# Performance work log

Measured on AMD Instinct MI355X. Metric: run time of the kernel, lower is better.

The kernel has to match this reference:

```python
import jax, jax.numpy as jnp
import numpy as np

B, S, D = 4, 2048, 1024
H, HD = 16, 64
L = 512          # kv latent dim (MLA compression)
E, TOPK, F = 8, 2, 2048  # MoE experts / top-k / expert hidden
EPS = 1e-6


def rmsnorm(x, g):
    return x * jax.lax.rsqrt(jnp.mean(x * x, axis=-1, keepdims=True) + EPS) * g


def setup_inputs() -> dict:
    key = jax.random.key(0)
    ks = jax.random.split(key, 16)
    std = 0.02
    inp = {
        "prev_hidden": jax.random.normal(ks[0], (B, S, D), jnp.float32),
        "future_token_embed": jax.random.normal(ks[1], (B, S, D), jnp.float32),
        "w_combine": jax.random.normal(ks[2], (2 * D, D), jnp.float32) * std,
        "g1": jnp.ones((D,), jnp.float32),
        "g2": jnp.ones((D,), jnp.float32),
        "g_attn": jnp.ones((D,), jnp.float32),
        "g_mlp": jnp.ones((D,), jnp.float32),
        "wq": jax.random.normal(ks[3], (D, D), jnp.float32) * std,
        "w_dkv": jax.random.normal(ks[4], (D, L), jnp.float32) * std,
        "w_uk": jax.random.normal(ks[5], (L, D), jnp.float32) * std,
        "w_uv": jax.random.normal(ks[6], (L, D), jnp.float32) * std,
        "wo": jax.random.normal(ks[7], (D, D), jnp.float32) * std,
        "w_gate": jax.random.normal(ks[8], (D, E), jnp.float32) * std,
        "w1": jax.random.normal(ks[9], (E, D, F), jnp.float32) * std,
        "w3": jax.random.normal(ks[10], (E, D, F), jnp.float32) * std,
        "w2": jax.random.normal(ks[11], (E, F, D), jnp.float32) * std,
    }
    return inp


def mla_attention(x, wq, w_dkv, w_uk, w_uv, wo):
    # Multi-head latent attention: KV compressed through latent dim L.
    q = (x @ wq).reshape(B, S, H, HD)
    c = x @ w_dkv                       # [B,S,L] latent
    k = (c @ w_uk).reshape(B, S, H, HD)
    v = (c @ w_uv).reshape(B, S, H, HD)
    scores = jnp.einsum("bqhd,bkhd->bhqk", q, k) / jnp.sqrt(jnp.float32(HD))
    causal = jnp.tril(jnp.ones((S, S), bool))
    scores = jnp.where(causal, scores, jnp.float32(-1e9))
    attn = jax.nn.softmax(scores, axis=-1)
    out = jnp.einsum("bhqk,bkhd->bqhd", attn, v).reshape(B, S, D)
    return out @ wo


def moe(x, w_gate, w1, w3, w2):
    t = x.reshape(-1, D)                          # [T,D]
    probs = jax.nn.softmax(t @ w_gate, axis=-1)   # [T,E]
    vals, idx = jax.lax.top_k(probs, TOPK)        # [T,K]
    vals = vals / jnp.sum(vals, axis=-1, keepdims=True)
    gates = jnp.sum(vals[:, :, None] * jax.nn.one_hot(idx, E, dtype=x.dtype), axis=1)  # [T,E]
    out = jnp.zeros_like(t)
    for e in range(E):  # fixed small expert loop (structurally distinct weights)
        h = jax.nn.silu(t @ w1[e]) * (t @ w3[e])
        out = out + gates[:, e:e + 1] * (h @ w2[e])
    return out.reshape(x.shape)


def reference(prev_hidden, future_token_embed, w_combine, g1, g2, g_attn, g_mlp,
              wq, w_dkv, w_uk, w_uv, wo, w_gate, w1, w3, w2):
    prev_norm = rmsnorm(prev_hidden, g1)
    future_norm = rmsnorm(future_token_embed, g2)
    combined = jnp.concatenate([prev_norm, future_norm], axis=-1)
    hidden = combined @ w_combine
    hidden = hidden + mla_attention(rmsnorm(hidden, g_attn), wq, w_dkv, w_uk, w_uv, wo)
    hidden = hidden + moe(rmsnorm(hidden, g_mlp), w_gate, w1, w3, w2)
    return hidden
```

## Files before the change

kernel.cpp:

```cpp
#include <hip/hip_runtime.h>
#include <hip/hip_bf16.h>
#include <stdint.h>

#define B_ 4
#define S_ 2048
#define D_ 1024
#define H_ 16
#define L_ 512
#define E_ 8
#define F_ 2048
#define T_ (B_*S_)

typedef __hip_bfloat16 bf16_t;
typedef __attribute__((ext_vector_type(8))) short short8;
typedef __attribute__((ext_vector_type(4))) float f32x4;

__device__ __forceinline__ void gl2lds16(const void* g, void* l) {
  __builtin_amdgcn_global_load_lds(
      reinterpret_cast<const __attribute__((address_space(1))) void*>(reinterpret_cast<uintptr_t>(g)),
      reinterpret_cast<__attribute__((address_space(3))) void*>(reinterpret_cast<uintptr_t>(l)),
      16, 0, 0);
}
__device__ __forceinline__ unsigned short bf16u(bf16_t b) {
  return *reinterpret_cast<unsigned short*>(&b);
}
__device__ __forceinline__ void split2(float v, bf16_t& ho, bf16_t& lo) {
  ho = __float2bfloat16(v);
  lo = __float2bfloat16(v - __bfloat162float(ho));
}
__device__ __forceinline__ float bf2f(bf16_t b) { return __bfloat162float(b); }

__global__ __launch_bounds__(256) void k_fill(float* out, float code, int n) {
  int i = blockIdx.x * 256 + threadIdx.x;
  if (i < n) out[i] = (i == 0 ? code : 0.f);
}

__global__ __launch_bounds__(256) void k_transpose(const float* __restrict__ in,
                                                   bf16_t* __restrict__ out, int R, int C, int ldin,
                                                   size_t zin, size_t zout) {
  __shared__ float t[32][33];
  const float* inz = in + (size_t)blockIdx.z * zin;
  bf16_t* outz = out + (size_t)blockIdx.z * zout;
  int c0 = blockIdx.x * 32, r0 = blockIdx.y * 32;
  int tx = threadIdx.x, ty = threadIdx.y;
#pragma unroll
  for (int i = 0; i < 4; ++i)
    t[ty + 8*i][tx] = inz[(size_t)(r0 + ty + 8*i) * ldin + c0 + tx];
  __syncthreads();
#pragma unroll
  for (int i = 0; i < 4; ++i)
    outz[(size_t)(c0 + ty + 8*i) * R + r0 + tx] = __float2bfloat16(t[tx][ty + 8*i]);
}

__global__ __launch_bounds__(256) void k_transpose2(const float* __restrict__ in,
                                                    bf16_t* __restrict__ oh, bf16_t* __restrict__ ol,
                                                    int R, int C, int ldin) {
  __shared__ float t[32][33];
  int c0 = blockIdx.x * 32, r0 = blockIdx.y * 32;
  int tx = threadIdx.x, ty = threadIdx.y;
#pragma unroll
  for (int i = 0; i < 4; ++i)
    t[ty + 8*i][tx] = in[(size_t)(r0 + ty + 8*i) * ldin + c0 + tx];
  __syncthreads();
#pragma unroll
  for (int i = 0; i < 4; ++i) {
    float v = t[tx][ty + 8*i];
    size_t idx = (size_t)(c0 + ty + 8*i) * R + r0 + tx;
    bf16_t h, l; split2(v, h, l);
    oh[idx] = h; ol[idx] = l;
  }
}

__global__ __launch_bounds__(256) void k_rms2cat2(const float* __restrict__ pa, const float* __restrict__ pb,
                                                  const float* __restrict__ g1, const float* __restrict__ g2,
                                                  bf16_t* __restrict__ oh, bf16_t* __restrict__ ol) {
  const int row = blockIdx.x, tid = threadIdx.x;
  float4 a = reinterpret_cast<const float4*>(pa + (size_t)row * D_)[tid];
  float4 b = reinterpret_cast<const float4*>(pb + (size_t)row * D_)[tid];
  float sa = a.x*a.x + a.y*a.y + a.z*a.z + a.w*a.w;
  float sb = b.x*b.x + b.y*b.y + b.z*b.z + b.w*b.w;
#pragma unroll
  for (int o = 32; o; o >>= 1) { sa += __shfl_xor(sa, o, 64); sb += __shfl_xor(sb, o, 64); }
  __shared__ float red[8];
  if ((tid & 63) == 0) { red[tid >> 6] = sa; red[4 + (tid >> 6)] = sb; }
  __syncthreads();
  sa = red[0] + red[1] + red[2] + red[3];
  sb = red[4] + red[5] + red[6] + red[7];
  float ra = rsqrtf(sa * (1.f / D_) + 1e-6f);
  float rb = rsqrtf(sb * (1.f / D_) + 1e-6f);
  float4 ga = reinterpret_cast<const float4*>(g1)[tid];
  float4 gb = reinterpret_cast<const float4*>(g2)[tid];
  float va[4] = {a.x*ra*ga.x, a.y*ra*ga.y, a.z*ra*ga.z, a.w*ra*ga.w};
  float vb[4] = {b.x*rb*gb.x, b.y*rb*gb.y, b.z*rb*gb.z, b.w*rb*gb.w};
  size_t base = (size_t)row * 2 * D_ + tid * 4;
#pragma unroll
  for (int j = 0; j < 4; ++j) {
    bf16_t h, l;
    split2(va[j], h, l); oh[base + j] = h; ol[base + j] = l;
    split2(vb[j], h, l); oh[base + D_ + j] = h; ol[base + D_ + j] = l;
  }
}

__global__ __launch_bounds__(256) void k_rmsnorm2(const float* __restrict__ x, const float* __restrict__ g,
                                                  bf16_t* __restrict__ oh, bf16_t* __restrict__ ol) {
  const int row = blockIdx.x, tid = threadIdx.x;
  float4 v = reinterpret_cast<const float4*>(x + (size_t)row * D_)[tid];
  float ss = v.x*v.x + v.y*v.y + v.z*v.z + v.w*v.w;
#pragma unroll
  for (int o = 32; o; o >>= 1) ss += __shfl_xor(ss, o, 64);
  __shared__ float red[4];
  if ((tid & 63) == 0) red[tid >> 6] = ss;
  __syncthreads();
  ss = red[0] + red[1] + red[2] + red[3];
  float rs = rsqrtf(ss * (1.f / D_) + 1e-6f);
  float4 gv = reinterpret_cast<const float4*>(g)[tid];
  float y[4] = {v.x*rs*gv.x, v.y*rs*gv.y, v.z*rs*gv.z, v.w*rs*gv.w};
  size_t base = (size_t)row * D_ + tid * 4;
#pragma unroll
  for (int j = 0; j < 4; ++j) {
    bf16_t h, l; split2(y[j], h, l);
    oh[base + j] = h;
    ol[base + j] = l;
  }
}

__global__ __launch_bounds__(256) void k_rmsgate(const float* __restrict__ x, const float* __restrict__ g,
                                                 const float* __restrict__ wg,
                                                 bf16_t* __restrict__ oh, float* __restrict__ gates) {
  const int row = blockIdx.x, tid = threadIdx.x;
  float4 v = reinterpret_cast<const float4*>(x + (size_t)row * D_)[tid];
  float ss = v.x*v.x + v.y*v.y + v.z*v.z + v.w*v.w;
#pragma unroll
  for (int o = 32; o; o >>= 1) ss += __shfl_xor(ss, o, 64);
  __shared__ float red[4];
  __shared__ float eacc[4][8];
  if ((tid & 63) == 0) red[tid >> 6] = ss;
  __syncthreads();
  ss = red[0] + red[1] + red[2] + red[3];
  float rs = rsqrtf(ss * (1.f / D_) + 1e-6f);
  float4 gv = reinterpret_cast<const float4*>(g)[tid];
  float y[4] = {v.x*rs*gv.x, v.y*rs*gv.y, v.z*rs*gv.z, v.w*rs*gv.w};
  size_t base = (size_t)row * D_ + tid * 4;
#pragma unroll
  for (int j = 0; j < 4; ++j) oh[base + j] = __float2bfloat16(y[j]);
  float acc[8] = {0, 0, 0, 0, 0, 0, 0, 0};
#pragma unroll
  for (int j = 0; j < 4; ++j) {
    const float* wgr = wg + (size_t)(tid * 4 + j) * 8;
#pragma unroll
    for (int e = 0; e < 8; ++e) acc[e] += y[j] * wgr[e];
  }
#pragma unroll
  for (int e = 0; e < 8; ++e) {
#pragma unroll
    for (int o = 32; o; o >>= 1) acc[e] += __shfl_xor(acc[e], o, 64);
  }
  if ((tid & 63) == 0) {
#pragma unroll
    for (int e = 0; e < 8; ++e) eacc[tid >> 6][e] = acc[e];
  }
  __syncthreads();
  if (tid == 0) {
    float a[8];
#pragma unroll
    for (int e = 0; e < 8; ++e) a[e] = eacc[0][e] + eacc[1][e] + eacc[2][e] + eacc[3][e];
    float mx = a[0];
#pragma unroll
    for (int e = 1; e < 8; ++e) mx = fmaxf(mx, a[e]);
    float p[8], sum = 0.f;
#pragma unroll
    for (int e = 0; e < 8; ++e) { p[e] = __expf(a[e] - mx); sum += p[e]; }
#pragma unroll
    for (int e = 0; e < 8; ++e) p[e] /= sum;
    int i0 = 0; float v0 = p[0];
#pragma unroll
    for (int e = 1; e < 8; ++e) if (p[e] > v0) { v0 = p[e]; i0 = e; }
    int i1 = -1; float v1 = -1.f;
#pragma unroll
    for (int e = 0; e < 8; ++e) if (e != i0 && p[e] > v1) { v1 = p[e]; i1 = e; }
    float norm = v0 + v1;
#pragma unroll
    for (int e = 0; e < 8; ++e)
      gates[(size_t)row * 8 + e] = (e == i0) ? v0 / norm : ((e == i1) ? v1 / norm : 0.f);
  }
}

__global__ __launch_bounds__(256) void k_route_det(const float* __restrict__ gates,
                                                   int* __restrict__ idx, int* __restrict__ cnt) {
  const int e = blockIdx.x, tid = threadIdx.x;
  __shared__ int sc[256];
  int base = 0;
  for (int c0 = 0; c0 < T_; c0 += 256) {
    int t = c0 + tid;
    int m = (gates[(size_t)t * 8 + e] > 0.f) ? 1 : 0;
    sc[tid] = m;
    __syncthreads();
#pragma unroll
    for (int off = 1; off < 256; off <<= 1) {
      int v = (tid >= off) ? sc[tid - off] : 0;
      __syncthreads();
      sc[tid] += v;
      __syncthreads();
    }
    if (m) idx[e * T_ + base + sc[tid] - 1] = t;
    int tot = sc[255];
    __syncthreads();
    base += tot;
  }
  if (tid == 0) cnt[e] = base;
}

__global__ void k_prefix(const int* __restrict__ cnt, int* __restrict__ off) {
  int s = 0;
  for (int e = 0; e < E_; ++e) { off[e] = s; s += cnt[e]; }
}

template <int EPI, int SPLIT, int IDX>
__global__ __launch_bounds__(256) void k_sgemm(
    const bf16_t* __restrict__ Ah, const bf16_t* __restrict__ Al,
    const bf16_t* __restrict__ Bh, const bf16_t* __restrict__ Bl,
    float* __restrict__ Cf, bf16_t* __restrict__ Cb, bf16_t* __restrict__ Cb2,
    bf16_t* __restrict__ Cb3, bf16_t* __restrict__ Cb4,
    const float* __restrict__ scale, const int* __restrict__ aidx, const int* __restrict__ cnt,
    int N, int K, int lda, int ldc) {
  __shared__ __align__(16) char lds[(SPLIT == 3 ? 4 : 2) * 16384];
  char* lsAh = lds;
  char* lsBh = lds + 16384;
  char* lsAl = lds + 32768;
  char* lsBl = lds + 49152;
  const int tid = threadIdx.x;
  const int l = tid & 63;
  const int g16 = l >> 4, c16 = l & 15;
  const int nbn = N >> 7;
  int swz = (int)blockIdx.x;
  if constexpr (IDX == 0 && EPI != 6) {
    swz = (swz & 7) * ((int)gridDim.x >> 3) + (swz >> 3);
  }
  const int bm = swz / nbn, bn = swz % nbn;
  const int m0 = bm << 7, n0 = bn << 7;
  const int w = tid >> 6;
  const int wr = w >> 1, wc = w & 1;

  int cval = 0;
  if constexpr (IDX == 1 || EPI == 6) {
    cval = *cnt;
    if (m0 >= cval) return;
  }

  f32x4 acc[4][4] = {};

  int Lb[4], sr[4], sk[4];
#pragma unroll
  for (int i = 0; i < 4; ++i) {
    Lb[i] = (tid + i * 256) * 16;
    sr[i] = Lb[i] >> 7;
    sk[i] = ((Lb[i] & 127) ^ ((sr[i] & 7) << 4)) >> 1;
  }
  int arow[4];
#pragma unroll
  for (int i = 0; i < 4; ++i) {
    if constexpr (IDX == 1) {
      int p = m0 + sr[i];
      arow[i] = aidx[p < cval ? p : cval - 1];
    } else {
      arow[i] = m0 + sr[i];
    }
  }

  for (int k0 = 0; k0 < K; k0 += 64) {
#pragma unroll
    for (int i = 0; i < 4; ++i) {
      size_t aoff = (size_t)arow[i] * lda + k0 + sk[i];
      size_t boff = (size_t)(n0 + sr[i]) * K + k0 + sk[i];
      gl2lds16(Ah + aoff, lsAh + Lb[i]);
      gl2lds16(Bh + boff, lsBh + Lb[i]);
      if constexpr (SPLIT == 3) {
        gl2lds16(Al + aoff, lsAl + Lb[i]);
        gl2lds16(Bl + boff, lsBl + Lb[i]);
      }
    }
    __syncthreads();
#pragma unroll
    for (int kc = 0; kc < 2; ++kc) {
      const int kb = (kc * 32 + 8 * g16) * 2;
      short8 afh[4], bfh[4], afl[4], bfl[4];
#pragma unroll
      for (int m = 0; m < 4; ++m) {
        int row = wr * 64 + m * 16 + c16;
        int off = row * 128 + (kb ^ ((row & 7) << 4));
        afh[m] = *reinterpret_cast<const short8*>(lsAh + off);
        if constexpr (SPLIT == 3) afl[m] = *reinterpret_cast<const short8*>(lsAl + off);
      }
#pragma unroll
      for (int n = 0; n < 4; ++n) {
        int row = wc * 64 + n * 16 + c16;
        int off = row * 128 + (kb ^ ((row & 7) << 4));
        bfh[n] = *reinterpret_cast<const short8*>(lsBh + off);
        if constexpr (SPLIT == 3) bfl[n] = *reinterpret_cast<const short8*>(lsBl + off);
      }
#pragma unroll
      for (int m = 0; m < 4; ++m)
#pragma unroll
        for (int n = 0; n < 4; ++n) {
          if constexpr (SPLIT == 3) {
            acc[m][n] = __builtin_amdgcn_mfma_f32_16x16x32_bf16(afl[m], bfh[n], acc[m][n], 0, 0, 0);
            acc[m][n] = __builtin_amdgcn_mfma_f32_16x16x32_bf16(afh[m], bfl[n], acc[m][n], 0, 0, 0);
          }
          acc[m][n] = __builtin_amdgcn_mfma_f32_16x16x32_bf16(afh[m], bfh[n], acc[m][n], 0, 0, 0);
        }
    }
    __syncthreads();
  }

#pragma unroll
  for (int m = 0; m < 4; ++m) {
    int rb = m0 + wr * 64 + m * 16 + 4 * g16;
#pragma unroll
    for (int n = 0; n < 4; ++n) {
      int gc = n0 + wc * 64 + n * 16 + c16;
#pragma unroll
      for (int r = 0; r < 4; ++r) {
        float v = acc[m][n][r];
        if constexpr (EPI == 6) {
          int rbr = rb + r;
          if (rbr < cval) {
            int tok = aidx[rbr];
            Cf[(size_t)tok * ldc + gc] += scale[(size_t)tok * 8] * v;
          }
        } else if constexpr (EPI == 7) {
          int t = rb + r;
          bf16_t h, lo; split2(v, h, lo);
          if (gc < 1024) {
            size_t ki = (size_t)t * 1024 + gc;
            Cb[ki] = h; Cb2[ki] = lo;
          } else {
            size_t vi = (size_t)(t >> 11) * 2097152 + (size_t)(gc - 1024) * 2048 + (t & 2047);
            Cb3[vi] = h; Cb4[vi] = lo;
          }
        } else {
          size_t idx = (size_t)(rb + r) * ldc + gc;
          if constexpr (EPI == 0) Cf[idx] = v;
          if constexpr (EPI == 1) Cf[idx] += v;
          if constexpr (EPI == 2) { bf16_t h, lo; split2(v, h, lo); Cb[idx] = h; Cb2[idx] = lo; }
          if constexpr (EPI == 3) Cb[idx] = __float2bfloat16(v / (1.f + __expf(-v)));
          if constexpr (EPI == 4) Cb[idx] = __float2bfloat16(bf2f(Cb[idx]) * v);
        }
      }
    }
  }
}

__global__ __launch_bounds__(256) void k_moe1(
    const bf16_t* __restrict__ xn, const bf16_t* __restrict__ w1t, const bf16_t* __restrict__ w3t,
    bf16_t* __restrict__ hg, const int* __restrict__ idx8, const int* __restrict__ cnt8,
    const int* __restrict__ off8) {
  __shared__ __align__(16) char lds[3 * 16384];
  char* lsA = lds;
  char* lsB1 = lds + 16384;
  char* lsB2 = lds + 32768;
  const int tid = threadIdx.x, l = tid & 63, g16 = l >> 4, c16 = l & 15;
  const int e = blockIdx.z;
  const int nbn = F_ >> 7;
  const int bm = (int)blockIdx.x / nbn, bn = (int)blockIdx.x % nbn;
  const int m0 = bm << 7, n0 = bn << 7;
  const int w = tid >> 6, wr = w >> 1, wc = w & 1;
  const int* aidx = idx8 + e * T_;
  const int cval = cnt8[e];
  if (m0 >= cval) return;
  const int obase = off8[e];
  const bf16_t* B1 = w1t + (size_t)e * D_ * F_;
  const bf16_t* B2 = w3t + (size_t)e * D_ * F_;

  f32x4 a1[4][4] = {}, a3[4][4] = {};
  int Lb[4], sr[4], sk[4], arow[4];
#pragma unroll
  for (int i = 0; i < 4; ++i) {
    Lb[i] = (tid + i * 256) * 16;
    sr[i] = Lb[i] >> 7;
    sk[i] = ((Lb[i] & 127) ^ ((sr[i] & 7) << 4)) >> 1;
    int p = m0 + sr[i];
    arow[i] = aidx[p < cval ? p : cval - 1];
  }
  for (int k0 = 0; k0 < D_; k0 += 64) {
#pragma unroll
    for (int i = 0; i < 4; ++i) {
      gl2lds16(xn + (size_t)arow[i] * D_ + k0 + sk[i], lsA + Lb[i]);
      size_t boff = (size_t)(n0 + sr[i]) * D_ + k0 + sk[i];
      gl2lds16(B1 + boff, lsB1 + Lb[i]);
      gl2lds16(B2 + boff, lsB2 + Lb[i]);
    }
    __syncthreads();
#pragma unroll
    for (int kc = 0; kc < 2; ++kc) {
      const int kb = (kc * 32 + 8 * g16) * 2;
      short8 af[4], b1[4], b2[4];
#pragma unroll
      for (int m = 0; m < 4; ++m) {
        int row = wr * 64 + m * 16 + c16;
        af[m] = *reinterpret_cast<const short8*>(lsA + row * 128 + (kb ^ ((row & 7) << 4)));
      }
#pragma unroll
      for (int n = 0; n < 4; ++n) {
        int row = wc * 64 + n * 16 + c16;
        int off = row * 128 + (kb ^ ((row & 7) << 4));
        b1[n] = *reinterpret_cast<const short8*>(lsB1 + off);
        b2[n] = *reinterpret_cast<const short8*>(lsB2 + off);
      }
#pragma unroll
      for (int m = 0; m < 4; ++m)
#pragma unroll
        for (int n = 0; n < 4; ++n) {
          a1[m][n] = __builtin_amdgcn_mfma_f32_16x16x32_bf16(af[m], b1[n], a1[m][n], 0, 0, 0);
          a3[m][n] = __builtin_amdgcn_mfma_f32_16x16x32_bf16(af[m], b2[n], a3[m][n], 0, 0, 0);
        }
    }
    __syncthreads();
  }
#pragma unroll
  for (int m = 0; m < 4; ++m) {
    int rb = m0 + wr * 64 + m * 16 + 4 * g16;
#pragma unroll
    for (int n = 0; n < 4; ++n) {
      int gc = n0 + wc * 64 + n * 16 + c16;
#pragma unroll
      for (int r = 0; r < 4; ++r) {
        int rbr = rb + r;
        if (rbr < cval) {
          float v1 = a1[m][n][r], v3 = a3[m][n][r];
          hg[(size_t)(obase + rbr) * F_ + gc] = __float2bfloat16(v1 / (1.f + __expf(-v1)) * v3);
        }
      }
    }
  }
}

__global__ __launch_bounds__(256) void k_moe2z(
    const bf16_t* __restrict__ hg, const bf16_t* __restrict__ w2t,
    float* __restrict__ hid, const float* __restrict__ gates,
    const int* __restrict__ idx8, const int* __restrict__ cnt8, const int* __restrict__ off8) {
  __shared__ __align__(16) char lds[2 * 16384];
  char* lsA = lds;
  char* lsB = lds + 16384;
  const int tid = threadIdx.x, l = tid & 63, g16 = l >> 4, c16 = l & 15;
  const int e = blockIdx.z;
  const int nbn = D_ >> 7;
  const int bm = (int)blockIdx.x / nbn, bn = (int)blockIdx.x % nbn;
  const int m0 = bm << 7, n0 = bn << 7;
  const int w = tid >> 6, wr = w >> 1, wc = w & 1;
  const int* aidx = idx8 + e * T_;
  const int cval = cnt8[e];
  if (m0 >= cval) return;
  const int obase = off8[e];
  const bf16_t* Bt = w2t + (size_t)e * D_ * F_;

  f32x4 acc[4][4] = {};
  int Lb[4], sr[4], sk[4];
#pragma unroll
  for (int i = 0; i < 4; ++i) {
    Lb[i] = (tid + i * 256) * 16;
    sr[i] = Lb[i] >> 7;
    sk[i] = ((Lb[i] & 127) ^ ((sr[i] & 7) << 4)) >> 1;
  }
  for (int k0 = 0; k0 < F_; k0 += 64) {
#pragma unroll
    for (int i = 0; i < 4; ++i) {
      gl2lds16(hg + (size_t)(obase + m0 + sr[i]) * F_ + k0 + sk[i], lsA + Lb[i]);
      gl2lds16(Bt + (size_t)(n0 + sr[i]) * F_ + k0 + sk[i], lsB + Lb[i]);
    }
    __syncthreads();
#pragma unroll
    for (int kc = 0; kc < 2; ++kc) {
      const int kb = (kc * 32 + 8 * g16) * 2;
      short8 af[4], bf8[4];
#pragma unroll
      for (int m = 0; m < 4; ++m) {
        int row = wr * 64 + m * 16 + c16;
        af[m] = *reinterpret_cast<const short8*>(lsA + row * 128 + (kb ^ ((row & 7) << 4)));
      }
#pragma unroll
      for (int n = 0; n < 4; ++n) {
        int row = wc * 64 + n * 16 + c16;
        bf8[n] = *reinterpret_cast<const short8*>(lsB + row * 128 + (kb ^ ((row & 7) << 4)));
      }
#pragma unroll
      for (int m = 0; m < 4; ++m)
#pragma unroll
        for (int n = 0; n < 4; ++n)
          acc[m][n] = __builtin_amdgcn_mfma_f32_16x16x32_bf16(af[m], bf8[n], acc[m][n], 0, 0, 0);
    }
    __syncthreads();
  }
#pragma unroll
  for (int m = 0; m < 4; ++m) {
    int rb = m0 + wr * 64 + m * 16 + 4 * g16;
#pragma unroll
    for (int n = 0; n < 4; ++n) {
      int gc = n0 + wc * 64 + n * 16 + c16;
#pragma unroll
      for (int r = 0; r < 4; ++r) {
        int rbr = rb + r;
        if (rbr < cval) {
          int tok = aidx[rbr];
          atomicAdd(&hid[(size_t)tok * D_ + gc], gates[(size_t)tok * 8 + e] * acc[m][n][r]);
        }
      }
    }
  }
}

__global__ __launch_bounds__(1024) void k_flash16(
    const bf16_t* __restrict__ qh, const bf16_t* __restrict__ ql,
    const bf16_t* __restrict__ kbh, const bf16_t* __restrict__ kbl,
    const bf16_t* __restrict__ vth, const bf16_t* __restrict__ vtl,
    bf16_t* __restrict__ ch, bf16_t* __restrict__ cl, int zb) {
  __shared__ __align__(16) char lds[131072];
  const int tid = threadIdx.x, l = tid & 63, w = tid >> 6;
  const int g16 = l >> 4, c16 = l & 15;
  const int qt = (int)gridDim.y - 1 - (int)blockIdx.y;
  const int h = (int)blockIdx.x / zb;
  const int z = (int)blockIdx.x % zb;
  const int zS = z * S_;
  const size_t vz = (size_t)z * 2097152;

  const int qrow = qt * 256 + w * 16 + c16;
  const size_t qoff = (size_t)(zS + qrow) * 1536 + h * 64 + 8 * g16;
  const short8 aq0h = *reinterpret_cast<const short8*>(qh + qoff);
  const short8 aq1h = *reinterpret_cast<const short8*>(qh + qoff + 32);
  const short8 aq0l = *reinterpret_cast<const short8*>(ql + qoff);
  const short8 aq1l = *reinterpret_cast<const short8*>(ql + qoff + 32);

  float mrow[4] = {-3e38f, -3e38f, -3e38f, -3e38f};
  float lrow[4] = {0.f, 0.f, 0.f, 0.f};
  f32x4 o[4] = {};
  char* Pwh = lds + 65536 + w * 2048;
  char* Pwl = lds + 98304 + w * 2048;

  auto stage = [&](int buf, int kt) {
    char* base = lds + buf * 32768;
    int t2 = tid & 511;
    int Lb = t2 * 16;
    int r = Lb >> 7;
    int dd = ((Lb & 127) ^ ((r & 7) << 4)) >> 1;
    if (tid < 512) {
      size_t ko = (size_t)(zS + kt * 64 + r) * 1024 + h * 64 + dd;
      gl2lds16(kbh + ko, base + Lb);
      gl2lds16(kbl + ko, base + 8192 + Lb);
    } else {
      size_t vo = vz + (size_t)(h * 64 + r) * 2048 + kt * 64 + dd;
      gl2lds16(vth + vo, base + 16384 + Lb);
      gl2lds16(vtl + vo, base + 24576 + Lb);
    }
  };

  const int nkt = 4 * qt + 4;
  stage(0, 0);
  for (int kt = 0; kt < nkt; ++kt) {
    const int cb = kt & 1;
    char* Kh = lds + cb * 32768;
    char* Kl = Kh + 8192;
    char* Vh = Kh + 16384;
    char* Vl = Kh + 24576;
    __syncthreads();
    if (kt + 1 < nkt) stage(cb ^ 1, kt + 1);

    f32x4 s[4] = {};
#pragma unroll
    for (int kc = 0; kc < 2; ++kc) {
      const short8 ah8 = kc ? aq1h : aq0h;
      const short8 al8 = kc ? aq1l : aq0l;
      const int kb = (kc * 32 + 8 * g16) * 2;
#pragma unroll
      for (int n = 0; n < 4; ++n) {
        int row = n * 16 + c16;
        int off = row * 128 + (kb ^ ((row & 7) << 4));
        short8 bkh = *reinterpret_cast<const short8*>(Kh + off);
        short8 bkl = *reinterpret_cast<const short8*>(Kl + off);
        s[n] = __builtin_amdgcn_mfma_f32_16x16x32_bf16(al8, bkh, s[n], 0, 0, 0);
        s[n] = __builtin_amdgcn_mfma_f32_16x16x32_bf16(ah8, bkl, s[n], 0, 0, 0);
        s[n] = __builtin_amdgcn_mfma_f32_16x16x32_bf16(ah8, bkh, s[n], 0, 0, 0);
      }
    }

    const bool dreg = (kt >= 4 * qt);
#pragma unroll
    for (int r = 0; r < 4; ++r) {
      const int rowabs = qt * 256 + w * 16 + 4 * g16 + r;
      float mx = -3e38f;
#pragma unroll
      for (int n = 0; n < 4; ++n) {
        float sv = s[n][r] * 0.125f;
        if (dreg && (kt * 64 + n * 16 + c16 > rowabs)) sv = -3e38f;
        s[n][r] = sv;
        mx = fmaxf(mx, sv);
      }
      mx = fmaxf(mx, __shfl_xor(mx, 1, 64));
      mx = fmaxf(mx, __shfl_xor(mx, 2, 64));
      mx = fmaxf(mx, __shfl_xor(mx, 4, 64));
      mx = fmaxf(mx, __shfl_xor(mx, 8, 64));
      float mnew = fmaxf(mrow[r], mx);
      float alpha = __expf(mrow[r] - mnew);
      float rsum = 0.f;
#pragma unroll
      for (int n = 0; n < 4; ++n) {
        float pp = __expf(s[n][r] - mnew);
        s[n][r] = pp;
        rsum += pp;
      }
      rsum += __shfl_xor(rsum, 1, 64);
      rsum += __shfl_xor(rsum, 2, 64);
      rsum += __shfl_xor(rsum, 4, 64);
      rsum += __shfl_xor(rsum, 8, 64);
      lrow[r] = lrow[r] * alpha + rsum;
      mrow[r] = mnew;
#pragma unroll
      for (int n = 0; n < 4; ++n) o[n][r] *= alpha;
    }

#pragma unroll
    for (int n = 0; n < 4; ++n)
#pragma unroll
      for (int r = 0; r < 4; ++r) {
        int row = 4 * g16 + r, col = n * 16 + c16;
        int off = row * 128 + ((col * 2) ^ ((row & 7) << 4));
        bf16_t ph, pl; split2(s[n][r], ph, pl);
        *reinterpret_cast<unsigned short*>(Pwh + off) = bf16u(ph);
        *reinterpret_cast<unsigned short*>(Pwl + off) = bf16u(pl);
      }

#pragma unroll
    for (int kc = 0; kc < 2; ++kc) {
      const int kb = (kc * 32 + 8 * g16) * 2;
      int poff = c16 * 128 + (kb ^ ((c16 & 7) << 4));
      short8 aph = *reinterpret_cast<const short8*>(Pwh + poff);
      short8 apl = *reinterpret_cast<const short8*>(Pwl + poff);
#pragma unroll
      for (int n = 0; n < 4; ++n) {
        int dr = n * 16 + c16;
        int off = dr * 128 + (kb ^ ((dr & 7) << 4));
        short8 bvh = *reinterpret_cast<const short8*>(Vh + off);
        short8 bvl = *reinterpret_cast<const short8*>(Vl + off);
        o[n] = __builtin_amdgcn_mfma_f32_16x16x32_bf16(apl, bvh, o[n], 0, 0, 0);
        o[n] = __builtin_amdgcn_mfma_f32_16x16x32_bf16(aph, bvl, o[n], 0, 0, 0);
        o[n] = __builtin_amdgcn_mfma_f32_16x16x32_bf16(aph, bvh, o[n], 0, 0, 0);
      }
    }
  }

#pragma unroll
  for (int n = 0; n < 4; ++n)
#pragma unroll
    for (int r = 0; r < 4; ++r) {
      float val = o[n][r] / lrow[r];
      size_t idx = (size_t)(zS + qt * 256 + w * 16 + 4 * g16 + r) * 1024 + h * 64 + n * 16 + c16;
      bf16_t hh, ll; split2(val, hh, ll);
      ch[idx] = hh; cl[idx] = ll;
    }
}

extern "C" void kernel_launch(void* const* d_in, const int* in_sizes, int n_in,
                              void* d_out, int out_size, void* d_ws, size_t ws_size,
                              hipStream_t stream) {
  const size_t MB = 1ull << 20;

  static const int dictSz[16] = {8388608, 8388608, 2097152, 1024, 1024, 1024, 1024,
                                 1048576, 524288, 524288, 524288, 1048576, 8192,
                                 16777216, 16777216, 16777216};
  static const int alphaSz[16] = {8388608, 1024, 1024, 1024, 1024, 8388608,
                                  16777216, 16777216, 16777216, 2097152, 524288,
                                  8192, 524288, 524288, 1048576, 1048576};
  bool isDict = (n_in == 16), isAlpha = (n_in == 16);
  for (int i = 0; i < 16; ++i) {
    if (n_in != 16) break;
    if (in_sizes[i] != dictSz[i]) isDict = false;
    if (in_sizes[i] != alphaSz[i]) isAlpha = false;
  }
  if ((!isDict && !isAlpha) || ws_size < 64 * MB) {
    k_fill<<<(out_size + 255) / 256, 256, 0, stream>>>((float*)d_out, 444.f, out_size);
    return;
  }

  const float *prev, *fut, *w_combine, *g1, *g2, *g_attn, *g_mlp, *wq, *w_dkv,
      *w_uk, *w_uv, *wo, *w_gate, *w1, *w3, *w2;
  if (isDict) {
    prev = (const float*)d_in[0];  fut = (const float*)d_in[1];
    w_combine = (const float*)d_in[2];
    g1 = (const float*)d_in[3];  g2 = (const float*)d_in[4];
    g_attn = (const float*)d_in[5];  g_mlp = (const float*)d_in[6];
    wq = (const float*)d_in[7];  w_dkv = (const float*)d_in[8];
    w_uk = (const float*)d_in[9];  w_uv = (const float*)d_in[10];
    wo = (const float*)d_in[11];  w_gate = (const float*)d_in[12];
    w1 = (const float*)d_in[13];  w3 = (const float*)d_in[14];
    w2 = (const float*)d_in[15];
  } else {
    fut = (const float*)d_in[0];
    g1 = (const float*)d_in[1];  g2 = (const float*)d_in[2];
    g_attn = (const float*)d_in[3];  g_mlp = (const float*)d_in[4];
    prev = (const float*)d_in[5];
    w1 = (const float*)d_in[6];  w2 = (const float*)d_in[7];  w3 = (const float*)d_in[8];
    w_combine = (const float*)d_in[9];  w_dkv = (const float*)d_in[10];
    w_gate = (const float*)d_in[11];  w_uk = (const float*)d_in[12];
    w_uv = (const float*)d_in[13];  wo = (const float*)d_in[14];
    wq = (const float*)d_in[15];
  }

  float* hid = (float*)d_out;
  char* ws = (char*)d_ws;
  const bool big = (ws_size >= 192 * MB);

  bf16_t* wcth = (bf16_t*)(ws + 0 * MB);
  bf16_t* wctl = (bf16_t*)(ws + 4 * MB);
  bf16_t* qcTh = (bf16_t*)(ws + 0 * MB);
  bf16_t* qcTl = (bf16_t*)(ws + 3 * MB);
  bf16_t* kvTh = (bf16_t*)(ws + 6 * MB);
  bf16_t* kvTl = (bf16_t*)(ws + 8 * MB);
  bf16_t* woth = (bf16_t*)(ws + 10 * MB);
  bf16_t* wotl = (bf16_t*)(ws + 12 * MB);
  bf16_t* w1t  = (bf16_t*)(ws + 0 * MB);
  bf16_t* w3t  = (bf16_t*)(ws + 4 * MB);
  bf16_t* w2t  = (bf16_t*)(ws + 8 * MB);
  float*  gates = (float*)(ws + 14 * MB);
  int*    idx   = (int*)(ws + 14 * MB + 262144);
  int*    cnt   = (int*)(ws + 14 * MB + 524288);
  int*    off   = (int*)(ws + 14 * MB + 524288 + 64);
  bf16_t* xnh = (bf16_t*)(ws + 15 * MB);

  dim3 tb(32, 8);

  if (big) {
    bf16_t* xcath = (bf16_t*)(ws + 15 * MB);
    bf16_t* xcatl = (bf16_t*)(ws + 47 * MB);
    bf16_t* xnbh  = (bf16_t*)(ws + 15 * MB);
    bf16_t* xnbl  = (bf16_t*)(ws + 31 * MB);
    bf16_t* qch   = (bf16_t*)(ws + 47 * MB);
    bf16_t* qcl   = (bf16_t*)(ws + 71 * MB);
    bf16_t* kbh   = (bf16_t*)(ws + 95 * MB);
    bf16_t* kbl   = (bf16_t*)(ws + 111 * MB);
    bf16_t* vth   = (bf16_t*)(ws + 127 * MB);
    bf16_t* vtl   = (bf16_t*)(ws + 143 * MB);
    bf16_t* ctxh  = (bf16_t*)(ws + 159 * MB);
    bf16_t* ctxl  = (bf16_t*)(ws + 175 * MB);
    bf16_t* hg    = (bf16_t*)(ws + 31 * MB);
    bf16_t* w1tA  = (bf16_t*)(ws + 95 * MB);
    bf16_t* w3tA  = (bf16_t*)(ws + 127 * MB);
    bf16_t* w2tA  = (bf16_t*)(ws + 159 * MB);

    k_transpose2<<<dim3(32, 64), tb, 0, stream>>>(w_combine, wcth, wctl, 2 * D_, D_, D_);
    k_rms2cat2<<<T_, 256, 0, stream>>>(prev, fut, g1, g2, xcath, xcatl);
    k_sgemm<0, 3, 0><<<dim3(64 * 8), 256, 0, stream>>>(
        xcath, xcatl, wcth, wctl, hid, nullptr, nullptr, nullptr, nullptr,
        nullptr, nullptr, nullptr, D_, 2 * D_, 2 * D_, D_);

    k_transpose2<<<dim3(32, 32), tb, 0, stream>>>(wq, qcTh, qcTl, D_, D_, D_);
    k_transpose2<<<dim3(16, 32), tb, 0, stream>>>(w_dkv, qcTh + 1024 * 1024, qcTl + 1024 * 1024, D_, L_, L_);
    k_transpose2<<<dim3(32, 16), tb, 0, stream>>>(w_uk, kvTh, kvTl, L_, D_, D_);
    k_transpose2<<<dim3(32, 16), tb, 0, stream>>>(w_uv, kvTh + 1024 * 512, kvTl + 1024 * 512, L_, D_, D_);
    k_transpose2<<<dim3(32, 32), tb, 0, stream>>>(wo, woth, wotl, D_, D_, D_);
    k_rmsnorm2<<<T_, 256, 0, stream>>>(hid, g_attn, xnbh, xnbl);
    k_sgemm<2, 3, 0><<<dim3(64 * 12), 256, 0, stream>>>(
        xnbh, xnbl, qcTh, qcTl, nullptr, qch, qcl, nullptr, nullptr,
        nullptr, nullptr, nullptr, 1536, D_, D_, 1536);
    k_sgemm<7, 3, 0><<<dim3(64 * 16), 256, 0, stream>>>(
        qch + 1024, qcl + 1024, kvTh, kvTl, nullptr, kbh, kbl, vth, vtl,
        nullptr, nullptr, nullptr, 2048, L_, 1536, 1024);
    k_flash16<<<dim3(H_ * B_, 8, 1), 1024, 0, stream>>>(qch, qcl, kbh, kbl, vth, vtl, ctxh, ctxl, B_);
    k_sgemm<1, 3, 0><<<dim3(64 * 8), 256, 0, stream>>>(
        ctxh, ctxl, woth, wotl, hid, nullptr, nullptr, nullptr, nullptr,
        nullptr, nullptr, nullptr, D_, D_, D_, D_);

    k_rmsgate<<<T_, 256, 0, stream>>>(hid, g_mlp, w_gate, xnh, gates);
    k_route_det<<<E_, 256, 0, stream>>>(gates, idx, cnt);
    k_prefix<<<1, 1, 0, stream>>>(cnt, off);
    k_transpose<<<dim3(64, 32, 8), tb, 0, stream>>>(w1, w1tA, D_, F_, F_, (size_t)D_ * F_, (size_t)F_ * D_);
    k_transpose<<<dim3(64, 32, 8), tb, 0, stream>>>(w3, w3tA, D_, F_, F_, (size_t)D_ * F_, (size_t)F_ * D_);
    k_transpose<<<dim3(32, 64, 8), tb, 0, stream>>>(w2, w2tA, F_, D_, D_, (size_t)F_ * D_, (size_t)D_ * F_);
    k_moe1<<<dim3(64 * 16, 1, 8), 256, 0, stream>>>(xnh, w1tA, w3tA, hg, idx, cnt, off);
    k_moe2z<<<dim3(64 * 8, 1, 8), 256, 0, stream>>>(hg, w2tA, hid, gates, idx, cnt, off);
  } else {
    bf16_t* xcath = (bf16_t*)(ws + 15 * MB);
    bf16_t* xcatl = (bf16_t*)(ws + 23 * MB);
    bf16_t* xnbh  = (bf16_t*)(ws + 15 * MB);
    bf16_t* xnbl  = (bf16_t*)(ws + 19 * MB);
    bf16_t* qch   = (bf16_t*)(ws + 23 * MB);
    bf16_t* qcl   = (bf16_t*)(ws + 29 * MB);
    bf16_t* kbh   = (bf16_t*)(ws + 35 * MB);
    bf16_t* kbl   = (bf16_t*)(ws + 39 * MB);
    bf16_t* vth   = (bf16_t*)(ws + 43 * MB);
    bf16_t* vtl   = (bf16_t*)(ws + 47 * MB);
    bf16_t* ctxh  = (bf16_t*)(ws + 51 * MB);
    bf16_t* ctxl  = (bf16_t*)(ws + 55 * MB);
    bf16_t* hg    = (bf16_t*)(ws + 31 * MB);

    k_transpose2<<<dim3(32, 64), tb, 0, stream>>>(w_combine, wcth, wctl, 2 * D_, D_, D_);
    for (int b = 0; b < B_; ++b) {
      size_t ro = (size_t)b * S_ * D_;
      k_rms2cat2<<<S_, 256, 0, stream>>>(prev + ro, fut + ro, g1, g2, xcath, xcatl);
      k_sgemm<0, 3, 0><<<dim3(16 * 8), 256, 0, stream>>>(
          xcath, xcatl, wcth, wctl, hid + ro, nullptr, nullptr, nullptr, nullptr,
          nullptr, nullptr, nullptr, D_, 2 * D_, 2 * D_, D_);
    }
    k_transpose2<<<dim3(32, 32), tb, 0, stream>>>(wq, qcTh, qcTl, D_, D_, D_);
    k_transpose2<<<dim3(16, 32), tb, 0, stream>>>(w_dkv, qcTh + 1024 * 1024, qcTl + 1024 * 1024, D_, L_, L_);
    k_transpose2<<<dim3(32, 16), tb, 0, stream>>>(w_uk, kvTh, kvTl, L_, D_, D_);
    k_transpose2<<<dim3(32, 16), tb, 0, stream>>>(w_uv, kvTh + 1024 * 512, kvTl + 1024 * 512, L_, D_, D_);
    k_transpose2<<<dim3(32, 32), tb, 0, stream>>>(wo, woth, wotl, D_, D_, D_);
    for (int b = 0; b < B_; ++b) {
      size_t ro = (size_t)b * S_ * D_;
      k_rmsnorm2<<<S_, 256, 0, stream>>>(hid + ro, g_attn, xnbh, xnbl);
      k_sgemm<2, 3, 0><<<dim3(16 * 12), 256, 0, stream>>>(
          xnbh, xnbl, qcTh, qcTl, nullptr, qch, qcl, nullptr, nullptr,
          nullptr, nullptr, nullptr, 1536, D_, D_, 1536);
      k_sgemm<7, 3, 0><<<dim3(16 * 16), 256, 0, stream>>>(
          qch + 1024, qcl + 1024, kvTh, kvTl, nullptr, kbh, kbl, vth, vtl,
          nullptr, nullptr, nullptr, 2048, L_, 1536, 1024);
      k_flash16<<<dim3(H_, 8, 1), 1024, 0, stream>>>(qch, qcl, kbh, kbl, vth, vtl, ctxh, ctxl, 1);
      k_sgemm<1, 3, 0><<<dim3(16 * 8), 256, 0, stream>>>(
          ctxh, ctxl, woth, wotl, hid + ro, nullptr, nullptr, nullptr, nullptr,
          nullptr, nullptr, nullptr, D_, D_, D_, D_);
    }
    k_rmsgate<<<T_, 256, 0, stream>>>(hid, g_mlp, w_gate, xnh, gates);
    k_route_det<<<E_, 256, 0, stream>>>(gates, idx, cnt);
    k_prefix<<<1, 1, 0, stream>>>(cnt, off);
    for (int e = 0; e < E_; ++e) {
      const int* ide = idx + e * T_;
      const int* cne = cnt + e;
      k_transpose<<<dim3(64, 32, 1), tb, 0, stream>>>(w1 + (size_t)e * D_ * F_, w1t, D_, F_, F_, 0, 0);
      k_transpose<<<dim3(64, 32, 1), tb, 0, stream>>>(w3 + (size_t)e * D_ * F_, w3t, D_, F_, F_, 0, 0);
      k_transpose<<<dim3(32, 64, 1), tb, 0, stream>>>(w2 + (size_t)e * F_ * D_, w2t, F_, D_, D_, 0, 0);
      k_sgemm<3, 1, 1><<<dim3(64 * 16), 256, 0, stream>>>(
          xnh, nullptr, w1t, nullptr, nullptr, hg, nullptr, nullptr, nullptr,
          nullptr, ide, cne, F_, D_, D_, F_);
      k_sgemm<4, 1, 1><<<dim3(64 * 16), 256, 0, stream>>>(
          xnh, nullptr, w3t, nullptr, nullptr, hg, nullptr, nullptr, nullptr,
          nullptr, ide, cne, F_, D_, D_, F_);
      k_sgemm<6, 1, 0><<<dim3(64 * 8), 256, 0, stream>>>(
          hg, nullptr, w2t, nullptr, hid, nullptr, nullptr, nullptr, nullptr,
          gates + e, ide, cne, D_, F_, F_, D_);
    }
  }
}
```

Baseline: 1.293 ms.

## Replace MoE down-projection atomics with bf16 staging and per-token gather sum

The second MoE GEMM now writes unscaled per-expert outputs as bf16 into a staging buffer instead of doing gated float atomicAdd into the hidden state. A new per-token kernel gathers the two selected expert rows through a position map recorded during routing, applies the gates, and adds them to the hidden state. This removes scattered atomic traffic and makes the summation order deterministic. The cost is an extra kernel launch, an extra round trip through memory, and rounding the expert outputs to bf16 before they are summed.

```diff
diff --git a/kernel.cpp b/kernel.cpp
--- a/kernel.cpp
+++ b/kernel.cpp
@@ -186,7 +186,8 @@
 }
 
 __global__ __launch_bounds__(256) void k_route_det(const float* __restrict__ gates,
-                                                   int* __restrict__ idx, int* __restrict__ cnt) {
+                                                   int* __restrict__ idx, int* __restrict__ cnt,
+                                                   int* __restrict__ pos8) {
   const int e = blockIdx.x, tid = threadIdx.x;
   __shared__ int sc[256];
   int base = 0;
@@ -202,7 +203,11 @@
       sc[tid] += v;
       __syncthreads();
     }
-    if (m) idx[e * T_ + base + sc[tid] - 1] = t;
+    if (m) {
+      int p = base + sc[tid] - 1;
+      idx[e * T_ + p] = t;
+      pos8[e * T_ + t] = p;
+    }
     int tot = sc[255];
     __syncthreads();
     base += tot;
@@ -213,6 +218,26 @@
 __global__ void k_prefix(const int* __restrict__ cnt, int* __restrict__ off) {
   int s = 0;
   for (int e = 0; e < E_; ++e) { off[e] = s; s += cnt[e]; }
+}
+
+__global__ __launch_bounds__(256) void k_moesum(float* __restrict__ hid, const bf16_t* __restrict__ hgo,
+                                                const float* __restrict__ gates,
+                                                const int* __restrict__ pos8, const int* __restrict__ off) {
+  const int t = blockIdx.x, tid = threadIdx.x;
+  size_t hbase = (size_t)t * D_ + tid * 4;
+  float4 acc = *reinterpret_cast<const float4*>(hid + hbase);
+#pragma unroll
+  for (int e = 0; e < 8; ++e) {
+    float g = gates[(size_t)t * 8 + e];
+    if (g > 0.f) {
+      size_t rb = (size_t)(off[e] + pos8[e * T_ + t]) * D_ + tid * 4;
+      acc.x += g * bf2f(hgo[rb + 0]);
+      acc.y += g * bf2f(hgo[rb + 1]);
+      acc.z += g * bf2f(hgo[rb + 2]);
+      acc.w += g * bf2f(hgo[rb + 3]);
+    }
+  }
+  *reinterpret_cast<float4*>(hid + hbase) = acc;
 }
 
 template <int EPI, int SPLIT, int IDX>
@@ -434,10 +459,10 @@
   }
 }
 
-__global__ __launch_bounds__(256) void k_moe2z(
+__global__ __launch_bounds__(256) void k_moe2w(
     const bf16_t* __restrict__ hg, const bf16_t* __restrict__ w2t,
-    float* __restrict__ hid, const float* __restrict__ gates,
-    const int* __restrict__ idx8, const int* __restrict__ cnt8, const int* __restrict__ off8) {
+    bf16_t* __restrict__ hgo,
+    const int* __restrict__ cnt8, const int* __restrict__ off8) {
   __shared__ __align__(16) char lds[2 * 16384];
   char* lsA = lds;
   char* lsB = lds + 16384;
@@ -447,7 +472,6 @@
   const int bm = (int)blockIdx.x / nbn, bn = (int)blockIdx.x % nbn;
   const int m0 = bm << 7, n0 = bn << 7;
   const int w = tid >> 6, wr = w >> 1, wc = w & 1;
-  const int* aidx = idx8 + e * T_;
   const int cval = cnt8[e];
   if (m0 >= cval) return;
   const int obase = off8[e];
@@ -499,10 +523,8 @@
 #pragma unroll
       for (int r = 0; r < 4; ++r) {
         int rbr = rb + r;
-        if (rbr < cval) {
-          int tok = aidx[rbr];
-          atomicAdd(&hid[(size_t)tok * D_ + gc], gates[(size_t)tok * 8 + e] * acc[m][n][r]);
-        }
+        if (rbr < cval)
+          hgo[(size_t)(obase + rbr) * D_ + gc] = __float2bfloat16(acc[m][n][r]);
       }
     }
   }
@@ -720,8 +742,9 @@
   bf16_t* w2t  = (bf16_t*)(ws + 8 * MB);
   float*  gates = (float*)(ws + 14 * MB);
   int*    idx   = (int*)(ws + 14 * MB + 262144);
-  int*    cnt   = (int*)(ws + 14 * MB + 524288);
-  int*    off   = (int*)(ws + 14 * MB + 524288 + 64);
+  int*    pos8  = (int*)(ws + 14 * MB + 524288);
+  int*    cnt   = (int*)(ws + 14 * MB + 786432);
+  int*    off   = (int*)(ws + 14 * MB + 786432 + 64);
   bf16_t* xnh = (bf16_t*)(ws + 15 * MB);
 
   dim3 tb(32, 8);
@@ -740,6 +763,7 @@
     bf16_t* ctxh  = (bf16_t*)(ws + 159 * MB);
     bf16_t* ctxl  = (bf16_t*)(ws + 175 * MB);
     bf16_t* hg    = (bf16_t*)(ws + 31 * MB);
+    bf16_t* hgo   = (bf16_t*)(ws + 95 * MB);
     bf16_t* w1tA  = (bf16_t*)(ws + 95 * MB);
     bf16_t* w3tA  = (bf16_t*)(ws + 127 * MB);
     bf16_t* w2tA  = (bf16_t*)(ws + 159 * MB);
@@ -768,13 +792,14 @@
         nullptr, nullptr, nullptr, D_, D_, D_, D_);
 
     k_rmsgate<<<T_, 256, 0, stream>>>(hid, g_mlp, w_gate, xnh, gates);
-    k_route_det<<<E_, 256, 0, stream>>>(gates, idx, cnt);
+    k_route_det<<<E_, 256, 0, stream>>>(gates, idx, cnt, pos8);
     k_prefix<<<1, 1, 0, stream>>>(cnt, off);
     k_transpose<<<dim3(64, 32, 8), tb, 0, stream>>>(w1, w1tA, D_, F_, F_, (size_t)D_ * F_, (size_t)F_ * D_);
     k_transpose<<<dim3(64, 32, 8), tb, 0, stream>>>(w3, w3tA, D_, F_, F_, (size_t)D_ * F_, (size_t)F_ * D_);
     k_transpose<<<dim3(32, 64, 8), tb, 0, stream>>>(w2, w2tA, F_, D_, D_, (size_t)F_ * D_, (size_t)D_ * F_);
     k_moe1<<<dim3(64 * 16, 1, 8), 256, 0, stream>>>(xnh, w1tA, w3tA, hg, idx, cnt, off);
-    k_moe2z<<<dim3(64 * 8, 1, 8), 256, 0, stream>>>(hg, w2tA, hid, gates, idx, cnt, off);
+    k_moe2w<<<dim3(64 * 8, 1, 8), 256, 0, stream>>>(hg, w2tA, hgo, cnt, off);
+    k_moesum<<<T_, 256, 0, stream>>>(hid, hgo, gates, pos8, off);
   } else {
     bf16_t* xcath = (bf16_t*)(ws + 15 * MB);
     bf16_t* xcatl = (bf16_t*)(ws + 23 * MB);
@@ -818,7 +843,7 @@
           nullptr, nullptr, nullptr, D_, D_, D_, D_);
     }
     k_rmsgate<<<T_, 256, 0, stream>>>(hid, g_mlp, w_gate, xnh, gates);
-    k_route_det<<<E_, 256, 0, stream>>>(gates, idx, cnt);
+    k_route_det<<<E_, 256, 0, stream>>>(gates, idx, cnt, pos8);
     k_prefix<<<1, 1, 0, stream>>>(cnt, off);
     for (int e = 0; e < E_; ++e) {
       const int* ide = idx + e * T_;
```

Result: faster. 1.168 ms (-9.7%).
